# Kernel tuning notes

Hardware: AMD Instinct MI355X
Metric: run time of the kernel (lower is better)

The kernel has to match this reference:

```python
import jax, jax.numpy as jnp
import numpy as np

HID = 256
N_LAYERS = 4
DT = 0.05
EPS = 1e-3
TMAX = 50


def setup_inputs() -> dict:
    key = jax.random.key(0)
    ks = jax.random.split(key, 7)
    B, S, D = 8, 1024, HID
    s1 = 1.0 / np.sqrt(D)      # fan_in = D for w_state / w_input
    s2 = 1.0 / np.sqrt(2 * D)  # fan_in = 2D for tau_gate linear
    x = jax.random.normal(ks[0], (B, S, D), dtype=jnp.float32)
    Ws = jax.random.uniform(ks[1], (N_LAYERS, D, D), jnp.float32, -s1, s1)
    bs = jax.random.uniform(ks[2], (N_LAYERS, D), jnp.float32, -s1, s1)
    Wi = jax.random.uniform(ks[3], (N_LAYERS, D, D), jnp.float32, -s1, s1)
    bi = jax.random.uniform(ks[4], (N_LAYERS, D), jnp.float32, -s1, s1)
    Wt = jax.random.uniform(ks[5], (N_LAYERS, D, 2 * D), jnp.float32, -s2, s2)
    bt = jax.random.uniform(ks[6], (N_LAYERS, D), jnp.float32, -s2, s2)
    return {"x": x, "Ws": Ws, "bs": bs, "Wi": Wi, "bi": bi, "Wt": Wt, "bt": bt}


def _run(x, Ws, bs, Wi, bi, Wt, bt):
    B, S, D = x.shape

    def layer_fn(cur_in, layer):
        h_prev, Ws_i, bs_i, Wi_i, bi_i, Wt_i, bt_i = layer
        combined = jnp.concatenate([cur_in, h_prev], axis=-1)          # [B,S,2D]
        tau = jax.nn.sigmoid(jnp.einsum('bsk,dk->bsd', combined, Wt_i) + bt_i)
        forcing = jnp.tanh(
            jnp.einsum('bsd,ed->bse', h_prev, Ws_i) + bs_i
            + jnp.einsum('bsd,ed->bse', cur_in, Wi_i) + bi_i
        )
        h_new = jnp.clip(h_prev + DT * (-h_prev / (tau + 1e-6) + forcing), -10.0, 10.0)
        delta = jnp.max(jnp.abs(h_new - h_prev))
        return h_new, (h_new, delta)

    @jax.checkpoint
    def step(carry, i):
        states, result, done = carry
        _, (new_states, deltas) = jax.lax.scan(
            layer_fn, x, (states, Ws, bs, Wi, bi, Wt, bt))
        converged = jnp.max(deltas) < EPS
        states = jnp.where(done, states, new_states)
        # torch returns loop index t at the first converging iteration, else TMAX
        result = jnp.where(done | ~converged, result, i)
        done = done | converged
        return (states, result, done), None

    init = (jnp.zeros((N_LAYERS, B, S, D), x.dtype),
            jnp.array(TMAX, jnp.int32),
            jnp.array(False))
    (states, result, _), _ = jax.lax.scan(step, init, jnp.arange(TMAX, dtype=jnp.int32))
    return states[-1], result


def reference(x, Ws, bs, Wi, bi, Wt, bt):
    return _run(x, Ws, bs, Wi, bi, Wt, bt)
```

## Files before the change

### kernel.cpp

```cpp
#include <hip/hip_runtime.h>
#include <math.h>

#define HID 256
#define TWOH 512
#define ROWS 8192
#define NLAYER 4
#define TMAX 50
#define DT 0.05f
#define EPSC 1e-3f

typedef __bf16 bf16;
typedef __bf16 bf16x8 __attribute__((ext_vector_type(8)));
typedef float f32x4 __attribute__((ext_vector_type(4)));

__global__ void pack_w_kernel(const float* __restrict__ Ws,
                              const float* __restrict__ Wi,
                              const float* __restrict__ Wt,
                              bf16* __restrict__ Wf) {
    int e = blockIdx.x * 256 + threadIdx.x;
    int j    = e & 7;
    int lane = (e >> 3) & 63;
    int nt   = (e >> 9) & 3;
    int ci   = (e >> 11) & 15;
    int wv   = (e >> 15) & 7;
    int L    = (e >> 18);
    int n = wv * 64 + nt * 16 + (lane & 15);
    int k = ci * 32 + (lane >> 4) * 8 + j;
    int d = n >> 1;
    float v;
    if ((n & 1) == 0) {
        v = Wt[(size_t)L * HID * TWOH + (size_t)d * TWOH + k];
    } else {
        v = (k < HID) ? Wi[(size_t)L * HID * HID + (size_t)d * HID + k]
                      : Ws[(size_t)L * HID * HID + (size_t)d * HID + (k - HID)];
    }
    Wf[e] = (bf16)v;
}

__global__ void pack_b_kernel(const float* __restrict__ bs,
                              const float* __restrict__ bi,
                              const float* __restrict__ bt,
                              float* __restrict__ bp) {
    int idx = blockIdx.x * 256 + threadIdx.x;
    int L = idx / TWOH;
    int n = idx % TWOH;
    int d = n >> 1;
    bp[idx] = ((n & 1) == 0) ? bt[L * HID + d]
                             : (bs[L * HID + d] + bi[L * HID + d]);
}

__global__ __launch_bounds__(512, 1) void persistent_kernel(
    const float* __restrict__ x,
    const bf16* __restrict__ Wf,
    const float* __restrict__ bp,
    float* __restrict__ deltas,
    float* __restrict__ out)
{
    __shared__ bf16 sX[32 * 256];
    __shared__ bf16 sH[NLAYER][32 * 256];
    __shared__ float2 sBias[NLAYER][256];
    __shared__ float sRed[8];

    const int tid  = threadIdx.x;
    const int lane = tid & 63;
    const int wv   = tid >> 6;
    const int l15  = lane & 15;
    const int quad = lane >> 4;
    const int w64  = wv * 64;
    const size_t rowbase = (size_t)blockIdx.x * 32;

    #pragma unroll
    for (int it = 0; it < 2; ++it) {
        int s = tid + it * 512;
        int r = s >> 5, seg = s & 31;
        const float* gx = x + (rowbase + r) * HID + seg * 8;
        float4 v0 = *(const float4*)gx;
        float4 v1 = *(const float4*)(gx + 4);
        bf16x8 o;
        o[0]=(bf16)v0.x; o[1]=(bf16)v0.y; o[2]=(bf16)v0.z; o[3]=(bf16)v0.w;
        o[4]=(bf16)v1.x; o[5]=(bf16)v1.y; o[6]=(bf16)v1.z; o[7]=(bf16)v1.w;
        int pseg = (seg & 24) | ((seg & 7) ^ (r & 7));
        *(bf16x8*)&sX[r * 256 + pseg * 8] = o;
    }
    {
        bf16x8 z = {};
        bf16* hflat = &sH[0][0];
        #pragma unroll
        for (int it = 0; it < 8; ++it)
            *(bf16x8*)&hflat[(size_t)(tid + it * 512) * 8] = z;
    }
    #pragma unroll
    for (int it = 0; it < 2; ++it) {
        int i = tid + it * 512;
        sBias[i >> 8][i & 255] = *(const float2*)(bp + (i >> 8) * TWOH + 2 * (i & 255));
    }

    __syncthreads();

    for (int t = 0; t < TMAX; ++t) {
        float dmax = 0.0f;
        for (int L = 0; L < NLAYER; ++L) {
            const bf16* Alo = (L == 0) ? sX : sH[L - 1];
            bf16*       Ahi = sH[L];
            const bf16* wb = Wf + ((size_t)(L * 8 + wv) * 32768) + (size_t)lane * 8;

            f32x4 acc[2][4];
            #pragma unroll
            for (int mt = 0; mt < 2; ++mt)
                #pragma unroll
                for (int nt = 0; nt < 4; ++nt)
                    acc[mt][nt] = (f32x4){0.f, 0.f, 0.f, 0.f};

            bf16x8 bb[3][4];
            #pragma unroll
            for (int pi = 0; pi < 3; ++pi)
                #pragma unroll
                for (int nt = 0; nt < 4; ++nt)
                    bb[pi][nt] = *(const bf16x8*)(wb + (size_t)(pi * 4 + nt) * 512);

            #pragma unroll
            for (int ci = 0; ci < 16; ++ci) {
                const int p = ci % 3;
                const bf16* Asrc = (ci < 8) ? Alo : Ahi;
                const int segb = (ci & 7) * 4 + quad;
                bf16x8 a[2];
                #pragma unroll
                for (int mt = 0; mt < 2; ++mt) {
                    int row  = mt * 16 + l15;
                    int pseg = (segb & 24) | ((segb & 7) ^ (row & 7));
                    a[mt] = *(const bf16x8*)&Asrc[row * 256 + pseg * 8];
                }
                #pragma unroll
                for (int mt = 0; mt < 2; ++mt)
                    #pragma unroll
                    for (int nt = 0; nt < 4; ++nt)
                        acc[mt][nt] = __builtin_amdgcn_mfma_f32_16x16x32_bf16(
                            a[mt], bb[p][nt], acc[mt][nt], 0, 0, 0);
                if (ci + 3 < 16) {
                    #pragma unroll
                    for (int nt = 0; nt < 4; ++nt)
                        bb[p][nt] = *(const bf16x8*)(wb + (size_t)((ci + 3) * 4 + nt) * 512);
                }
            }

            __syncthreads();

            {
                const int odd = lane & 1;
                #pragma unroll
                for (int nt = 0; nt < 4; ++nt) {
                    const int d = (w64 + nt * 16 + l15) >> 1;
                    const float2 bb2 = sBias[L][d];
                    #pragma unroll
                    for (int mt = 0; mt < 2; ++mt) {
                        f32x4 v = acc[mt][nt];
                        float pp[4];
                        #pragma unroll
                        for (int r = 0; r < 4; ++r) pp[r] = __shfl_xor(v[r], 1);
                        #pragma unroll
                        for (int rr = 0; rr < 2; ++rr) {
                            const int r = (odd ? 2 : 0) + rr;
                            float tpre = (odd ? pp[r] : v[r]) + bb2.x;
                            float fpre = (odd ? v[r] : pp[r]) + bb2.y;
                            tpre = fminf(30.f, fmaxf(-30.f, tpre));
                            fpre = fminf(15.f, fmaxf(-15.f, fpre));
                            float u   = __expf(-tpre);
                            float den = 1.0f + 1e-6f + 1e-6f * u;
                            float rcp = __builtin_amdgcn_rcpf(den);
                            float e2  = __expf(2.0f * fpre);
                            float r2  = __builtin_amdgcn_rcpf(e2 + 1.0f);
                            float fo  = (e2 - 1.0f) * r2;
                            const int row = mt * 16 + quad * 4 + r;
                            const int seg = d >> 3;
                            const int idx = row * 256 +
                                (((seg & 24) | ((seg & 7) ^ (row & 7))) << 3) + (d & 7);
                            float h  = (float)Ahi[idx];
                            float g  = h * (1.0f + u) * rcp;
                            float nv = h + DT * (fo - g);
                            nv = fminf(10.0f, fmaxf(-10.0f, nv));
                            Ahi[idx] = (bf16)nv;
                            dmax = fmaxf(dmax, fabsf(nv - h));
                        }
                    }
                }
            }
            if (L == NLAYER - 1) {
                #pragma unroll
                for (int off = 32; off > 0; off >>= 1)
                    dmax = fmaxf(dmax, __shfl_xor(dmax, off));
                if (lane == 0) sRed[wv] = dmax;
            }
            __syncthreads();
        }

        if (tid == 0) {
            float m = sRed[0];
            #pragma unroll
            for (int w = 1; w < 8; ++w) m = fmaxf(m, sRed[w]);
            atomicMax((unsigned int*)(deltas + t), __float_as_uint(m));
        }
    }

    #pragma unroll
    for (int it = 0; it < 2; ++it) {
        int s = tid + it * 512;
        int r = s >> 5, seg = s & 31;
        int pseg = (seg & 24) | ((seg & 7) ^ (r & 7));
        bf16x8 v = *(const bf16x8*)&sH[NLAYER - 1][r * 256 + pseg * 8];
        float* go = out + (rowbase + r) * HID + seg * 8;
        float4 o0 = {(float)v[0], (float)v[1], (float)v[2], (float)v[3]};
        float4 o1 = {(float)v[4], (float)v[5], (float)v[6], (float)v[7]};
        *(float4*)go = o0;
        *(float4*)(go + 4) = o1;
    }
}

__global__ void result_kernel(const float* __restrict__ deltas,
                              float* __restrict__ out) {
    if (threadIdx.x == 0) {
        int res = TMAX;
        for (int t = 0; t < TMAX; ++t) {
            if (deltas[t] < EPSC) { res = t; break; }
        }
        out[(size_t)ROWS * HID] = (float)res;
    }
}

extern "C" void kernel_launch(void* const* d_in, const int* in_sizes, int n_in,
                              void* d_out, int out_size, void* d_ws, size_t ws_size,
                              hipStream_t stream) {
    const float* x  = (const float*)d_in[0];
    const float* Ws = (const float*)d_in[1];
    const float* bs = (const float*)d_in[2];
    const float* Wi = (const float*)d_in[3];
    const float* bi = (const float*)d_in[4];
    const float* Wt = (const float*)d_in[5];
    const float* bt = (const float*)d_in[6];
    float* out = (float*)d_out;

    char* p = (char*)d_ws;
    bf16*  Wf     = (bf16*)p;  p += (size_t)NLAYER * TWOH * TWOH * sizeof(bf16);
    float* bp     = (float*)p; p += (size_t)NLAYER * TWOH * sizeof(float);
    float* deltas = (float*)p; p += 64 * sizeof(float);

    hipMemsetAsync(deltas, 0, 64 * sizeof(float), stream);
    pack_w_kernel<<<(NLAYER * TWOH * TWOH) / 256, 256, 0, stream>>>(Ws, Wi, Wt, Wf);
    pack_b_kernel<<<(NLAYER * TWOH) / 256, 256, 0, stream>>>(bs, bi, bt, bp);

    persistent_kernel<<<256, 512, 0, stream>>>(x, Wf, bp, deltas, out);
    result_kernel<<<1, 64, 0, stream>>>(deltas, out);
}
```

Baseline: 1.344 ms.

## Switch weights and hidden states to FP8 MFMA with regrouped output columns

Replaces bf16 storage and bf16 MFMA with FP8 (e4m3) for weights, input and hidden states, using the fp8 16x16x32 MFMA. This halves weight bandwidth and LDS traffic, and deepens the weight prefetch ring to four stages. The weight packing now places tau and forcing columns in separate tiles instead of interleaving them, so the epilogue no longer needs lane shuffles. Keeping the recurrent state in FP8 sharply reduces precision, which risks accuracy failures and can change the convergence behaviour of the delta check.

```diff
diff --git a/kernel.cpp b/kernel.cpp
--- a/kernel.cpp
+++ b/kernel.cpp
@@ -9,14 +9,20 @@
 #define DT 0.05f
 #define EPSC 1e-3f
 
-typedef __bf16 bf16;
-typedef __bf16 bf16x8 __attribute__((ext_vector_type(8)));
 typedef float f32x4 __attribute__((ext_vector_type(4)));
+typedef unsigned char u8;
+
+__device__ inline u8 f32_to_fp8(float v) {
+    return (u8)(__builtin_amdgcn_cvt_pk_fp8_f32(v, v, 0, 0) & 0xff);
+}
+__device__ inline float fp8_to_f32(u8 b) {
+    return __builtin_amdgcn_cvt_f32_fp8((int)b, 0);
+}
 
 __global__ void pack_w_kernel(const float* __restrict__ Ws,
                               const float* __restrict__ Wi,
                               const float* __restrict__ Wt,
-                              bf16* __restrict__ Wf) {
+                              u8* __restrict__ Wf) {
     int e = blockIdx.x * 256 + threadIdx.x;
     int j    = e & 7;
     int lane = (e >> 3) & 63;
@@ -24,17 +30,18 @@
     int ci   = (e >> 11) & 15;
     int wv   = (e >> 15) & 7;
     int L    = (e >> 18);
-    int n = wv * 64 + nt * 16 + (lane & 15);
-    int k = ci * 32 + (lane >> 4) * 8 + j;
-    int d = n >> 1;
+    int l15  = lane & 15;
+    int quad = lane >> 4;
+    int d = wv * 32 + (nt & 1) * 16 + l15;
+    int k = ci * 32 + quad * 8 + j;
     float v;
-    if ((n & 1) == 0) {
+    if ((nt >> 1) == 0) {
         v = Wt[(size_t)L * HID * TWOH + (size_t)d * TWOH + k];
     } else {
         v = (k < HID) ? Wi[(size_t)L * HID * HID + (size_t)d * HID + k]
                       : Ws[(size_t)L * HID * HID + (size_t)d * HID + (k - HID)];
     }
-    Wf[e] = (bf16)v;
+    Wf[e] = f32_to_fp8(v);
 }
 
 __global__ void pack_b_kernel(const float* __restrict__ bs,
@@ -51,13 +58,13 @@
 
 __global__ __launch_bounds__(512, 1) void persistent_kernel(
     const float* __restrict__ x,
-    const bf16* __restrict__ Wf,
+    const u8* __restrict__ Wf,
     const float* __restrict__ bp,
     float* __restrict__ deltas,
     float* __restrict__ out)
 {
-    __shared__ bf16 sX[32 * 256];
-    __shared__ bf16 sH[NLAYER][32 * 256];
+    __shared__ u8 sX[32 * 256];
+    __shared__ u8 sH[NLAYER][32 * 256];
     __shared__ float2 sBias[NLAYER][256];
     __shared__ float sRed[8];
 
@@ -66,7 +73,7 @@
     const int wv   = tid >> 6;
     const int l15  = lane & 15;
     const int quad = lane >> 4;
-    const int w64  = wv * 64;
+    const int w32  = wv * 32;
     const size_t rowbase = (size_t)blockIdx.x * 32;
 
     #pragma unroll
@@ -76,18 +83,17 @@
         const float* gx = x + (rowbase + r) * HID + seg * 8;
         float4 v0 = *(const float4*)gx;
         float4 v1 = *(const float4*)(gx + 4);
-        bf16x8 o;
-        o[0]=(bf16)v0.x; o[1]=(bf16)v0.y; o[2]=(bf16)v0.z; o[3]=(bf16)v0.w;
-        o[4]=(bf16)v1.x; o[5]=(bf16)v1.y; o[6]=(bf16)v1.z; o[7]=(bf16)v1.w;
-        int pseg = (seg & 24) | ((seg & 7) ^ (r & 7));
-        *(bf16x8*)&sX[r * 256 + pseg * 8] = o;
+        int lo = __builtin_amdgcn_cvt_pk_fp8_f32(v0.x, v0.y, 0, 0);
+        lo     = __builtin_amdgcn_cvt_pk_fp8_f32(v0.z, v0.w, lo, 1);
+        int hi = __builtin_amdgcn_cvt_pk_fp8_f32(v1.x, v1.y, 0, 0);
+        hi     = __builtin_amdgcn_cvt_pk_fp8_f32(v1.z, v1.w, hi, 1);
+        long pk = ((long)(unsigned int)lo) | ((long)hi << 32);
+        *(long*)&sX[r * 256 + (seg ^ r) * 8] = pk;
     }
     {
-        bf16x8 z = {};
-        bf16* hflat = &sH[0][0];
+        long* hflat = (long*)&sH[0][0];
         #pragma unroll
-        for (int it = 0; it < 8; ++it)
-            *(bf16x8*)&hflat[(size_t)(tid + it * 512) * 8] = z;
+        for (int it = 0; it < 8; ++it) hflat[tid + it * 512] = 0;
     }
     #pragma unroll
     for (int it = 0; it < 2; ++it) {
@@ -100,9 +106,9 @@
     for (int t = 0; t < TMAX; ++t) {
         float dmax = 0.0f;
         for (int L = 0; L < NLAYER; ++L) {
-            const bf16* Alo = (L == 0) ? sX : sH[L - 1];
-            bf16*       Ahi = sH[L];
-            const bf16* wb = Wf + ((size_t)(L * 8 + wv) * 32768) + (size_t)lane * 8;
+            const u8* Alo = (L == 0) ? sX : sH[L - 1];
+            u8*       Ahi = sH[L];
+            const u8* wb = Wf + ((size_t)(L * 8 + wv) * 32768) + (size_t)lane * 8;
 
             f32x4 acc[2][4];
             #pragma unroll
@@ -111,76 +117,66 @@
                 for (int nt = 0; nt < 4; ++nt)
                     acc[mt][nt] = (f32x4){0.f, 0.f, 0.f, 0.f};
 
-            bf16x8 bb[3][4];
-            #pragma unroll
-            for (int pi = 0; pi < 3; ++pi)
+            long bb[4][4];
+            #pragma unroll
+            for (int pi = 0; pi < 4; ++pi)
                 #pragma unroll
                 for (int nt = 0; nt < 4; ++nt)
-                    bb[pi][nt] = *(const bf16x8*)(wb + (size_t)(pi * 4 + nt) * 512);
+                    bb[pi][nt] = *(const long*)(wb + (size_t)(pi * 4 + nt) * 512);
 
             #pragma unroll
             for (int ci = 0; ci < 16; ++ci) {
-                const int p = ci % 3;
-                const bf16* Asrc = (ci < 8) ? Alo : Ahi;
-                const int segb = (ci & 7) * 4 + quad;
-                bf16x8 a[2];
+                const int p = ci & 3;
+                const u8* Asrc = (ci < 8) ? Alo : Ahi;
+                const int seg = (ci & 7) * 4 + quad;
+                long a[2];
                 #pragma unroll
                 for (int mt = 0; mt < 2; ++mt) {
-                    int row  = mt * 16 + l15;
-                    int pseg = (segb & 24) | ((segb & 7) ^ (row & 7));
-                    a[mt] = *(const bf16x8*)&Asrc[row * 256 + pseg * 8];
+                    int row = mt * 16 + l15;
+                    a[mt] = *(const long*)&Asrc[row * 256 + (seg ^ row) * 8];
                 }
                 #pragma unroll
                 for (int mt = 0; mt < 2; ++mt)
                     #pragma unroll
                     for (int nt = 0; nt < 4; ++nt)
-                        acc[mt][nt] = __builtin_amdgcn_mfma_f32_16x16x32_bf16(
+                        acc[mt][nt] = __builtin_amdgcn_mfma_f32_16x16x32_fp8_fp8(
                             a[mt], bb[p][nt], acc[mt][nt], 0, 0, 0);
-                if (ci + 3 < 16) {
+                if (ci + 4 < 16) {
                     #pragma unroll
                     for (int nt = 0; nt < 4; ++nt)
-                        bb[p][nt] = *(const bf16x8*)(wb + (size_t)((ci + 3) * 4 + nt) * 512);
+                        bb[p][nt] = *(const long*)(wb + (size_t)((ci + 4) * 4 + nt) * 512);
                 }
             }
 
             __syncthreads();
 
-            {
-                const int odd = lane & 1;
-                #pragma unroll
-                for (int nt = 0; nt < 4; ++nt) {
-                    const int d = (w64 + nt * 16 + l15) >> 1;
-                    const float2 bb2 = sBias[L][d];
+            #pragma unroll
+            for (int ntp = 0; ntp < 2; ++ntp) {
+                const int d = w32 + ntp * 16 + l15;
+                const float2 bb2 = sBias[L][d];
+                const int seg = d >> 3, dlow = d & 7;
+                #pragma unroll
+                for (int mt = 0; mt < 2; ++mt) {
                     #pragma unroll
-                    for (int mt = 0; mt < 2; ++mt) {
-                        f32x4 v = acc[mt][nt];
-                        float pp[4];
-                        #pragma unroll
-                        for (int r = 0; r < 4; ++r) pp[r] = __shfl_xor(v[r], 1);
-                        #pragma unroll
-                        for (int rr = 0; rr < 2; ++rr) {
-                            const int r = (odd ? 2 : 0) + rr;
-                            float tpre = (odd ? pp[r] : v[r]) + bb2.x;
-                            float fpre = (odd ? v[r] : pp[r]) + bb2.y;
-                            tpre = fminf(30.f, fmaxf(-30.f, tpre));
-                            fpre = fminf(15.f, fmaxf(-15.f, fpre));
-                            float u   = __expf(-tpre);
-                            float den = 1.0f + 1e-6f + 1e-6f * u;
-                            float rcp = __builtin_amdgcn_rcpf(den);
-                            float e2  = __expf(2.0f * fpre);
-                            float r2  = __builtin_amdgcn_rcpf(e2 + 1.0f);
-                            float fo  = (e2 - 1.0f) * r2;
-                            const int row = mt * 16 + quad * 4 + r;
-                            const int seg = d >> 3;
-                            const int idx = row * 256 +
-                                (((seg & 24) | ((seg & 7) ^ (row & 7))) << 3) + (d & 7);
-                            float h  = (float)Ahi[idx];
-                            float g  = h * (1.0f + u) * rcp;
-                            float nv = h + DT * (fo - g);
-                            nv = fminf(10.0f, fmaxf(-10.0f, nv));
-                            Ahi[idx] = (bf16)nv;
-                            dmax = fmaxf(dmax, fabsf(nv - h));
-                        }
+                    for (int r = 0; r < 4; ++r) {
+                        float tpre = acc[mt][ntp][r]     + bb2.x;
+                        float fpre = acc[mt][ntp + 2][r] + bb2.y;
+                        tpre = fminf(30.f, fmaxf(-30.f, tpre));
+                        fpre = fminf(15.f, fmaxf(-15.f, fpre));
+                        float u   = __expf(-tpre);
+                        float den = 1.0f + 1e-6f + 1e-6f * u;
+                        float rcp = __builtin_amdgcn_rcpf(den);
+                        float e2  = __expf(2.0f * fpre);
+                        float r2  = __builtin_amdgcn_rcpf(e2 + 1.0f);
+                        float fo  = (e2 - 1.0f) * r2;
+                        const int row = mt * 16 + quad * 4 + r;
+                        const int idx = row * 256 + (seg ^ row) * 8 + dlow;
+                        float h  = fp8_to_f32(Ahi[idx]);
+                        float g  = h * (1.0f + u) * rcp;
+                        float nv = h + DT * (fo - g);
+                        nv = fminf(10.0f, fmaxf(-10.0f, nv));
+                        Ahi[idx] = f32_to_fp8(nv);
+                        dmax = fmaxf(dmax, fabsf(nv - h));
                     }
                 }
             }
@@ -205,11 +201,19 @@
     for (int it = 0; it < 2; ++it) {
         int s = tid + it * 512;
         int r = s >> 5, seg = s & 31;
-        int pseg = (seg & 24) | ((seg & 7) ^ (r & 7));
-        bf16x8 v = *(const bf16x8*)&sH[NLAYER - 1][r * 256 + pseg * 8];
+        long v = *(const long*)&sH[NLAYER - 1][r * 256 + (seg ^ r) * 8];
+        int lo = (int)(v & 0xffffffffl);
+        int hi = (int)(v >> 32);
         float* go = out + (rowbase + r) * HID + seg * 8;
-        float4 o0 = {(float)v[0], (float)v[1], (float)v[2], (float)v[3]};
-        float4 o1 = {(float)v[4], (float)v[5], (float)v[6], (float)v[7]};
+        float4 o0, o1;
+        o0.x = __builtin_amdgcn_cvt_f32_fp8(lo, 0);
+        o0.y = __builtin_amdgcn_cvt_f32_fp8(lo, 1);
+        o0.z = __builtin_amdgcn_cvt_f32_fp8(lo, 2);
+        o0.w = __builtin_amdgcn_cvt_f32_fp8(lo, 3);
+        o1.x = __builtin_amdgcn_cvt_f32_fp8(hi, 0);
+        o1.y = __builtin_amdgcn_cvt_f32_fp8(hi, 1);
+        o1.z = __builtin_amdgcn_cvt_f32_fp8(hi, 2);
+        o1.w = __builtin_amdgcn_cvt_f32_fp8(hi, 3);
         *(float4*)go = o0;
         *(float4*)(go + 4) = o1;
     }
@@ -239,7 +243,7 @@
     float* out = (float*)d_out;
 
     char* p = (char*)d_ws;
-    bf16*  Wf     = (bf16*)p;  p += (size_t)NLAYER * TWOH * TWOH * sizeof(bf16);
+    u8*    Wf     = (u8*)p;    p += (size_t)NLAYER * TWOH * TWOH;
     float* bp     = (float*)p; p += (size_t)NLAYER * TWOH * sizeof(float);
     float* deltas = (float*)p; p += 64 * sizeof(float);
 
```

After: 1.227 ms. 8.7% less time.
